# Optimization experiments

Measured on AMD Instinct MI355X. Metric: run time of the kernel, lower is better.

## Reference

```python
import math
import jax, jax.numpy as jnp
import numpy as np

B, S, D, H = 4, 2048, 1024, 16
HD = D // H
SAMPLING_FACTOR = 5.0


def setup_inputs() -> dict:
    key = jax.random.key(0)
    ks = jax.random.split(key, 6)
    std = 1.0 / math.sqrt(D)
    inp = {
        "x": jax.random.normal(ks[0], (B, S, D), dtype=jnp.float32),
        "Wq": jax.random.normal(ks[1], (D, D), dtype=jnp.float32) * std,
        "bq": jnp.zeros((D,), dtype=jnp.float32),
        "Wk": jax.random.normal(ks[2], (D, D), dtype=jnp.float32) * std,
        "bk": jnp.zeros((D,), dtype=jnp.float32),
        "Wv": jax.random.normal(ks[3], (D, D), dtype=jnp.float32) * std,
        "bv": jnp.zeros((D,), dtype=jnp.float32),
        "Wo": jax.random.normal(ks[4], (D, D), dtype=jnp.float32) * std,
        "bo": jnp.zeros((D,), dtype=jnp.float32),
        "sample_idx": jax.random.randint(ks[5], (S,), 0, S, dtype=jnp.int32),
    }
    return inp


def reference(x, Wq, bq, Wk, bk, Wv, bv, Wo, bo, sample_idx):
    batch, seq_len, d_model = x.shape
    scale = math.sqrt(HD)
    # u = number of top (active) queries; U_part = seq_len here (sampling saturates)
    u = max(1, min(seq_len, int(SAMPLING_FACTOR * math.log(seq_len + 1))))

    def proj(W, b):
        # [B,S,D] -> [B,H,S,hd]
        return (x @ W + b).reshape(batch, seq_len, H, HD).transpose(0, 2, 1, 3)

    Q = proj(Wq, bq)
    K = proj(Wk, bk)
    V = proj(Wv, bv)

    # sparsity measure over sampled keys (with replacement)
    K_sample = K[:, :, sample_idx, :]                     # [B,H,U,hd]
    scores_sample = jnp.einsum("bhsd,bhud->bhsu", Q, K_sample) / scale
    M = scores_sample.max(axis=-1) - scores_sample.mean(axis=-1)  # [B,H,S]

    _, top_idx = jax.lax.top_k(M, u)                      # [B,H,u]

    Q_reduce = jnp.take_along_axis(Q, top_idx[..., None], axis=2)  # [B,H,u,hd]
    attn_scores = jnp.einsum("bhud,bhsd->bhus", Q_reduce, K) / scale
    attn_probs = jax.nn.softmax(attn_scores, axis=-1)
    context = jnp.einsum("bhus,bhsd->bhud", attn_probs, V)        # [B,H,u,hd]

    # fill lazy queries with mean of V, scatter active-query contexts
    V_mean = V.mean(axis=2, keepdims=True)                # [B,H,1,hd]
    out = jnp.broadcast_to(V_mean, (batch, H, seq_len, HD))
    b_idx = jnp.arange(batch)[:, None, None]
    h_idx = jnp.arange(H)[None, :, None]
    out = out.at[b_idx, h_idx, top_idx].set(context)      # [B,H,S,hd]

    out = out.transpose(0, 2, 1, 3).reshape(batch, seq_len, d_model)
    return out @ Wo + bo
```

## Files before the change

### kernel.cpp

```cpp
#include <hip/hip_runtime.h>
#include <math.h>
#include <stdint.h>
#include <stddef.h>

#define BB 4
#define SS 2048
#define DD 1024
#define HH 16
#define HD 64
#define UU 38
#define BH (BB*HH)
#define NROWS (BB*SS)
#define QSZ (BB*HH*SS*HD)
#define NSPLIT 16
#define SPLEN (SS/NSPLIT)
#define QPAD 40

typedef unsigned short ushortT;
typedef unsigned int u32;
typedef __attribute__((ext_vector_type(8))) short bf16x8;
typedef __attribute__((ext_vector_type(4))) float f32x4;

static __device__ __forceinline__ ushortT f2bf(float f) {
  union { float f; unsigned int u; } v; v.f = f;
  unsigned int r = v.u + 0x7fffu + ((v.u >> 16) & 1u);
  return (ushortT)(r >> 16);
}
static __device__ __forceinline__ float bf2f(ushortT h) {
  union { unsigned int u; float f; } v; v.u = ((unsigned int)h) << 16; return v.f;
}
static __device__ __forceinline__ void gld16(const void* g, void* l) {
  __builtin_amdgcn_global_load_lds((const __attribute__((address_space(1))) u32*)g,
                                   (__attribute__((address_space(3))) u32*)l, 16, 0, 0);
}

__global__ __launch_bounds__(256) void split_x(
    const float* __restrict__ x, ushortT* __restrict__ xh, ushortT* __restrict__ xl)
{
  size_t i = ((size_t)blockIdx.x * 256 + threadIdx.x) * 8;
  float4 v0 = *(const float4*)&x[i];
  float4 v1 = *(const float4*)&x[i + 4];
  float fv[8] = {v0.x, v0.y, v0.z, v0.w, v1.x, v1.y, v1.z, v1.w};
  bf16x8 hv, lv;
#pragma unroll
  for (int j = 0; j < 8; ++j) {
    ushortT h = f2bf(fv[j]);
    hv[j] = (short)h;
    lv[j] = (short)f2bf(fv[j] - bf2f(h));
  }
  *(bf16x8*)&xh[i] = hv;
  *(bf16x8*)&xl[i] = lv;
}

__global__ __launch_bounds__(256) void splitT_kernel(
    const float* __restrict__ W, ushortT* __restrict__ WhT, ushortT* __restrict__ WlT)
{
  __shared__ float tile[64][65];
  const int t = threadIdx.x;
  const int bk = blockIdx.y * 64, bn = blockIdx.x * 64;
  const int rr = t >> 4, c4 = (t & 15) * 4;
#pragma unroll
  for (int p = 0; p < 4; ++p) {
    int row = rr + p * 16;
    float4 v = *(const float4*)&W[(size_t)(bk + row) * DD + bn + c4];
    tile[row][c4] = v.x; tile[row][c4+1] = v.y; tile[row][c4+2] = v.z; tile[row][c4+3] = v.w;
  }
  __syncthreads();
  const int n = t & 63, ks = (t >> 6) * 16;
  union { ushortT us[16]; uint4 q[2]; } hb, lb;
#pragma unroll
  for (int j = 0; j < 16; ++j) {
    float f = tile[ks + j][n];
    ushortT h = f2bf(f);
    hb.us[j] = h;
    lb.us[j] = f2bf(f - bf2f(h));
  }
  size_t o = ((size_t)(bn + n) * DD + (size_t)(bk + ks)) >> 3;
  ((uint4*)WhT)[o] = hb.q[0]; ((uint4*)WhT)[o + 1] = hb.q[1];
  ((uint4*)WlT)[o] = lb.q[0]; ((uint4*)WlT)[o + 1] = lb.q[1];
}

__global__ __launch_bounds__(256) void dedupe_kernel(
    const int* __restrict__ sidx, int* __restrict__ uidx, int* __restrict__ ucount)
{
  __shared__ unsigned bm[64];
  __shared__ int base[64];
  const int t = threadIdx.x;
  if (t < 64) bm[t] = 0;
  __syncthreads();
  for (int s = t; s < SS; s += 256) {
    int v = sidx[s];
    atomicOr(&bm[v >> 5], 1u << (v & 31));
  }
  __syncthreads();
  if (t < 64) {
    int c = __popc(bm[t]);
    int pre = c;
#pragma unroll
    for (int off = 1; off < 64; off <<= 1) {
      int o = __shfl_up(pre, off, 64);
      if (t >= off) pre += o;
    }
    base[t] = pre - c;
    if (t == 63) ucount[0] = pre;
  }
  __syncthreads();
  if (t < 64) {
    unsigned m = bm[t];
    int o = base[t];
    while (m) {
      int b = __ffs(m) - 1;
      uidx[o++] = t * 32 + b;
      m &= m - 1;
    }
  }
  __syncthreads();
  int total = ucount[0];
  int padded = (total + 127) & ~127;
  int first = uidx[0];
  for (int i = total + t; i < padded; i += 256) uidx[i] = first;
}

__global__ __launch_bounds__(256, 4) void gemm_qkv(
    const ushortT* __restrict__ Axh, const ushortT* __restrict__ Axl,
    const ushortT* __restrict__ WqhT, const ushortT* __restrict__ WqlT,
    const ushortT* __restrict__ WkhT, const ushortT* __restrict__ WklT,
    const ushortT* __restrict__ WvhT, const ushortT* __restrict__ WvlT,
    const float* __restrict__ bq, const float* __restrict__ bk, const float* __restrict__ bv,
    ushortT* __restrict__ Qhg, ushortT* __restrict__ Qlg,
    ushortT* __restrict__ Khg, ushortT* __restrict__ Klg,
    float* __restrict__ V)
{
  __shared__ ushortT As[128 * 64];
  __shared__ ushortT Bs[128 * 64];
  const int t = threadIdx.x;
  const int lin = blockIdx.x;
  const int xcd = lin & 7;
  const int idx = lin >> 3;
  const int msub = idx & 3;
  const int rest = idx >> 2;
  const int n_idx = rest % 24;
  const int half = rest / 24;
  const int m_loc = half * 4 + msub;
  const int m0 = (xcd * 8 + m_loc) * 128;
  const int p = n_idx >> 3;
  const int n0 = (n_idx & 7) * 128;
  const ushortT* Bh = (p == 0) ? WqhT : (p == 1) ? WkhT : WvhT;
  const ushortT* Bl = (p == 0) ? WqlT : (p == 1) ? WklT : WvlT;
  const float* bias = (p == 0) ? bq : (p == 1) ? bk : bv;
  const int lane = t & 63, w = t >> 6;
  const int wr = w >> 1, wc = w & 1;
  const int fr = lane & 15, fs = lane >> 4;
  const int srow = t >> 3, sslot = t & 7;
  f32x4 acc[4][4];
#pragma unroll
  for (int i = 0; i < 4; ++i)
#pragma unroll
    for (int j = 0; j < 4; ++j) acc[i][j] = (f32x4){0.f, 0.f, 0.f, 0.f};

  for (int kt = 0; kt < 48; ++kt) {
    const int seg = kt >> 4;
    const int rk0 = (kt & 15) * 64;
    const ushortT* a_src = (seg == 1) ? Axl : Axh;
    const ushortT* b_src = (seg == 2) ? Bl : Bh;
    __syncthreads();
#pragma unroll
    for (int is = 0; is < 4; ++is) {
      int row = is * 32 + srow;
      int soff = ((sslot ^ (row & 7)) * 8);
      int cb = (is * 256 + (t & 192)) * 8;
      gld16(&a_src[(size_t)(m0 + row) * DD + rk0 + soff], &As[cb]);
      gld16(&b_src[(size_t)(n0 + row) * DD + rk0 + soff], &Bs[cb]);
    }
    __syncthreads();
#pragma unroll
    for (int kk = 0; kk < 2; ++kk) {
      bf16x8 af[4], bf[4];
#pragma unroll
      for (int i = 0; i < 4; ++i) {
        int row = wr * 64 + i * 16 + fr;
        af[i] = *(const bf16x8*)&As[row * 64 + (((kk * 4 + fs) ^ (row & 7)) * 8)];
      }
#pragma unroll
      for (int j = 0; j < 4; ++j) {
        int row = wc * 64 + j * 16 + fr;
        bf[j] = *(const bf16x8*)&Bs[row * 64 + (((kk * 4 + fs) ^ (row & 7)) * 8)];
      }
#pragma unroll
      for (int i = 0; i < 4; ++i)
#pragma unroll
        for (int j = 0; j < 4; ++j)
          acc[i][j] = __builtin_amdgcn_mfma_f32_16x16x32_bf16(af[i], bf[j], acc[i][j], 0, 0, 0);
    }
  }
#pragma unroll
  for (int i = 0; i < 4; ++i) {
#pragma unroll
    for (int j = 0; j < 4; ++j) {
      int c = n0 + wc * 64 + j * 16 + fr;
      float bs = bias[c];
      int h = c >> 6, hd = c & 63;
#pragma unroll
      for (int r = 0; r < 4; ++r) {
        int m = m0 + wr * 64 + i * 16 + fs * 4 + r;
        int b = m >> 11, s = m & (SS - 1);
        size_t oidx = (((size_t)(b * HH + h)) * SS + s) * HD + hd;
        float val = acc[i][j][r] + bs;
        if (p == 2) {
          V[oidx] = val;
        } else {
          ushortT hv = f2bf(val);
          ushortT lv = f2bf(val - bf2f(hv));
          if (p == 0) { Qhg[oidx] = hv; Qlg[oidx] = lv; }
          else        { Khg[oidx] = hv; Klg[oidx] = lv; }
        }
      }
    }
  }
}

__global__ __launch_bounds__(256) void means_kernel(
    const ushortT* __restrict__ Khg, const ushortT* __restrict__ Klg,
    const float* __restrict__ V, const int* __restrict__ sidx,
    float* __restrict__ Kmean, float* __restrict__ Vmean)
{
  __shared__ float rk[4][64], rv[4][64];
  const int bh = blockIdx.x;
  const int t = threadIdx.x;
  const int d = t & 63, p = t >> 6;
  const float* Vb = V + (size_t)bh * SS * HD;
  float ka = 0.f, va = 0.f;
  for (int r = p * 512; r < (p + 1) * 512; ++r) {
    size_t ki = ((size_t)bh * SS + sidx[r]) * HD + d;
    ka += bf2f(Khg[ki]) + bf2f(Klg[ki]);
    va += Vb[(size_t)r * HD + d];
  }
  rk[p][d] = ka; rv[p][d] = va;
  __syncthreads();
  if (t < 64) {
    Kmean[bh * HD + t] = (rk[0][t] + rk[1][t] + rk[2][t] + rk[3][t]) * (1.0f / SS);
    Vmean[bh * HD + t] = (rv[0][t] + rv[1][t] + rv[2][t] + rv[3][t]) * (1.0f / SS);
  }
}

__global__ __launch_bounds__(256, 3) void m_mfma(
    const ushortT* __restrict__ Qhg, const ushortT* __restrict__ Qlg,
    const ushortT* __restrict__ Khg, const ushortT* __restrict__ Klg,
    const int* __restrict__ uidx, const int* __restrict__ ucount,
    const float* __restrict__ Kmean, float* __restrict__ M)
{
  __shared__ ushortT KhL[128 * 64], KlL[128 * 64];
  __shared__ float Mred[2][128];
  __shared__ float km[64];
  const int t = threadIdx.x;
  const int lin = blockIdx.x;
  const int swz = (lin & 7) * 128 + (lin >> 3);
  const int bh = swz >> 4;
  const int s0 = (swz & 15) * 128;
  const int lane = t & 63, w = t >> 6;
  const int wr = w >> 1, wc = w & 1;
  const int fr = lane & 15, fs = lane >> 4;
  if (t < 64) km[t] = Kmean[bh * HD + t];
  const int srow = t >> 3, sslot = t & 7;
  const int ntiles = (ucount[0] + 127) >> 7;
  const size_t qbase = (size_t)bh * SS + s0;
  float runmax[4][4];
#pragma unroll
  for (int i = 0; i < 4; ++i)
#pragma unroll
    for (int r = 0; r < 4; ++r) runmax[i][r] = -INFINITY;

  for (int ui = 0; ui < ntiles; ++ui) {
    __syncthreads();
#pragma unroll
    for (int is = 0; is < 4; ++is) {
      int row = is * 32 + srow;
      int gr = uidx[ui * 128 + row];
      int soff = ((sslot ^ (row & 7)) * 8);
      int cb = (is * 256 + (t & 192)) * 8;
      size_t ga = ((size_t)bh * SS + gr) * HD + soff;
      gld16(&Khg[ga], &KhL[cb]);
      gld16(&Klg[ga], &KlL[cb]);
    }
    __syncthreads();
    f32x4 acc[4][4];
#pragma unroll
    for (int i = 0; i < 4; ++i)
#pragma unroll
      for (int j = 0; j < 4; ++j) acc[i][j] = (f32x4){0.f, 0.f, 0.f, 0.f};
#pragma unroll
    for (int kk = 0; kk < 2; ++kk) {
      bf16x8 ah[4], al[4], bh[4], bl[4];
#pragma unroll
      for (int i = 0; i < 4; ++i) {
        size_t ga = (qbase + (size_t)(wr * 64 + i * 16 + fr)) * HD + kk * 32 + fs * 8;
        ah[i] = *(const bf16x8*)&Qhg[ga];
        al[i] = *(const bf16x8*)&Qlg[ga];
      }
#pragma unroll
      for (int j = 0; j < 4; ++j) {
        int row = wc * 64 + j * 16 + fr;
        int off = row * 64 + (((kk * 4 + fs) ^ (row & 7)) * 8);
        bh[j] = *(const bf16x8*)&KhL[off];
        bl[j] = *(const bf16x8*)&KlL[off];
      }
#pragma unroll
      for (int i = 0; i < 4; ++i)
#pragma unroll
        for (int j = 0; j < 4; ++j) {
          acc[i][j] = __builtin_amdgcn_mfma_f32_16x16x32_bf16(ah[i], bh[j], acc[i][j], 0, 0, 0);
          acc[i][j] = __builtin_amdgcn_mfma_f32_16x16x32_bf16(ah[i], bl[j], acc[i][j], 0, 0, 0);
          acc[i][j] = __builtin_amdgcn_mfma_f32_16x16x32_bf16(al[i], bh[j], acc[i][j], 0, 0, 0);
        }
    }
#pragma unroll
    for (int i = 0; i < 4; ++i)
#pragma unroll
      for (int j = 0; j < 4; ++j)
#pragma unroll
        for (int r = 0; r < 4; ++r) runmax[i][r] = fmaxf(runmax[i][r], acc[i][j][r]);
  }
#pragma unroll
  for (int i = 0; i < 4; ++i)
#pragma unroll
    for (int r = 0; r < 4; ++r) {
      float v = runmax[i][r];
      v = fmaxf(v, __shfl_xor(v, 1, 64));
      v = fmaxf(v, __shfl_xor(v, 2, 64));
      v = fmaxf(v, __shfl_xor(v, 4, 64));
      v = fmaxf(v, __shfl_xor(v, 8, 64));
      runmax[i][r] = v;
    }
  if (fr == 0) {
#pragma unroll
    for (int i = 0; i < 4; ++i)
#pragma unroll
      for (int r = 0; r < 4; ++r)
        Mred[wc][wr * 64 + i * 16 + fs * 4 + r] = runmax[i][r];
  }
  __syncthreads();
  if (t < 128) {
    float mx = fmaxf(Mred[0][t], Mred[1][t]);
    float md = 0.f;
    const ushortT* qh = &Qhg[(qbase + t) * HD];
    const ushortT* ql = &Qlg[(qbase + t) * HD];
#pragma unroll
    for (int k8 = 0; k8 < 8; ++k8) {
      bf16x8 hv = *(const bf16x8*)&qh[k8 * 8];
      bf16x8 lv = *(const bf16x8*)&ql[k8 * 8];
#pragma unroll
      for (int j = 0; j < 8; ++j)
        md += (bf2f((ushortT)hv[j]) + bf2f((ushortT)lv[j])) * km[k8 * 8 + j];
    }
    M[(size_t)bh * SS + s0 + t] = (mx - md) * 0.125f;
  }
}

__global__ __launch_bounds__(256) void topk_kernel(const float* __restrict__ M,
                                                   int* __restrict__ topi)
{
  __shared__ float rw[4];
  __shared__ int   ri4[4];
  __shared__ int   winner;
  const int t = threadIdx.x, bh = blockIdx.x;
  const int lane = t & 63, w = t >> 6;
  float v[8];
#pragma unroll
  for (int j = 0; j < 8; ++j) v[j] = M[(size_t)bh * SS + t + j * 256];
  for (int it = 0; it < UU; ++it) {
    float bv = v[0]; int bj = 0;
#pragma unroll
    for (int j = 1; j < 8; ++j) if (v[j] > bv) { bv = v[j]; bj = j; }
    int bs = t + bj * 256;
#pragma unroll
    for (int off = 32; off > 0; off >>= 1) {
      float ov = __shfl_xor(bv, off, 64);
      int os = __shfl_xor(bs, off, 64);
      if (ov > bv || (ov == bv && os < bs)) { bv = ov; bs = os; }
    }
    if (lane == 0) { rw[w] = bv; ri4[w] = bs; }
    __syncthreads();
    if (t == 0) {
      float fv = rw[0]; int fsx = ri4[0];
#pragma unroll
      for (int g = 1; g < 4; ++g)
        if (rw[g] > fv || (rw[g] == fv && ri4[g] < fsx)) { fv = rw[g]; fsx = ri4[g]; }
      topi[bh * UU + it] = fsx;
      winner = fsx;
    }
    __syncthreads();
    int wi = winner;
    if ((wi & 255) == t) {
      int jj = wi >> 8;
#pragma unroll
      for (int j = 0; j < 8; ++j) if (j == jj) v[j] = -INFINITY;
    }
  }
}

__global__ __launch_bounds__(256) void attn_flash(
    const ushortT* __restrict__ Qhg, const ushortT* __restrict__ Qlg,
    const ushortT* __restrict__ Khg, const ushortT* __restrict__ Klg,
    const float* __restrict__ V, const int* __restrict__ topi,
    float* __restrict__ pacc, float* __restrict__ pm, float* __restrict__ pl)
{
  __shared__ float Qt[64][68];
  __shared__ float KV[64][68];
  __shared__ float Ps[64][68];
  __shared__ float redA[16][64];
  __shared__ float redB[16][64];
  __shared__ float mrow[64], lrow[64], scl[64];
  const int t  = threadIdx.x;
  const int bh = blockIdx.x;
  const int sp = blockIdx.y;
  const float* Vb = V + (size_t)bh * SS * HD;
  if (t < 64) { mrow[t] = -INFINITY; lrow[t] = 0.f; }
  {
    int q = t >> 2, k4 = (t & 3) * 16;
    float fv[16];
#pragma unroll
    for (int e = 0; e < 16; ++e) fv[e] = 0.f;
    if (q < UU) {
      int qidx = topi[bh * UU + q];
      size_t ga = ((size_t)bh * SS + qidx) * HD + k4;
      bf16x8 h0 = *(const bf16x8*)&Qhg[ga];
      bf16x8 h1 = *(const bf16x8*)&Qhg[ga + 8];
      bf16x8 l0 = *(const bf16x8*)&Qlg[ga];
      bf16x8 l1 = *(const bf16x8*)&Qlg[ga + 8];
#pragma unroll
      for (int j = 0; j < 8; ++j) {
        fv[j]     = bf2f((ushortT)h0[j]) + bf2f((ushortT)l0[j]);
        fv[8 + j] = bf2f((ushortT)h1[j]) + bf2f((ushortT)l1[j]);
      }
    }
#pragma unroll
    for (int e = 0; e < 16; ++e) Qt[k4 + e][q] = fv[e];
  }
  const int q4 = (t & 15) * 4, j4g = (t >> 4) * 4, d4 = (t >> 4) * 4;
  const int lj = t >> 2, lk4 = (t & 3) * 16;
  float acc[4][4] = {};
  for (int s0 = sp * SPLEN; s0 < (sp + 1) * SPLEN; s0 += 64) {
    __syncthreads();
    {
      size_t ga = ((size_t)bh * SS + s0 + lj) * HD + lk4;
      bf16x8 h0 = *(const bf16x8*)&Khg[ga];
      bf16x8 h1 = *(const bf16x8*)&Khg[ga + 8];
      bf16x8 l0 = *(const bf16x8*)&Klg[ga];
      bf16x8 l1 = *(const bf16x8*)&Klg[ga + 8];
#pragma unroll
      for (int j = 0; j < 8; ++j) {
        KV[lk4 + j][lj]     = bf2f((ushortT)h0[j]) + bf2f((ushortT)l0[j]);
        KV[lk4 + 8 + j][lj] = bf2f((ushortT)h1[j]) + bf2f((ushortT)l1[j]);
      }
    }
    __syncthreads();
    float sacc[4][4] = {};
#pragma unroll 16
    for (int k = 0; k < 64; ++k) {
      float4 a = *(const float4*)&Qt[k][q4];
      float4 b = *(const float4*)&KV[k][j4g];
      sacc[0][0] += a.x*b.x; sacc[0][1] += a.x*b.y; sacc[0][2] += a.x*b.z; sacc[0][3] += a.x*b.w;
      sacc[1][0] += a.y*b.x; sacc[1][1] += a.y*b.y; sacc[1][2] += a.y*b.z; sacc[1][3] += a.y*b.w;
      sacc[2][0] += a.z*b.x; sacc[2][1] += a.z*b.y; sacc[2][2] += a.z*b.z; sacc[2][3] += a.z*b.w;
      sacc[3][0] += a.w*b.x; sacc[3][1] += a.w*b.y; sacc[3][2] += a.w*b.z; sacc[3][3] += a.w*b.w;
    }
#pragma unroll
    for (int i = 0; i < 4; ++i) {
      float mx = fmaxf(fmaxf(sacc[i][0], sacc[i][1]), fmaxf(sacc[i][2], sacc[i][3]));
      redA[t >> 4][q4 + i] = mx;
    }
    __syncthreads();
    if (t < 64) {
      float mx = redA[0][t];
#pragma unroll
      for (int g = 1; g < 16; ++g) mx = fmaxf(mx, redA[g][t]);
      float mn = fmaxf(mrow[t], mx * 0.125f);
      scl[t] = __expf(mrow[t] - mn);
      mrow[t] = mn;
    }
    __syncthreads();
    float4 vld[4];
#pragma unroll
    for (int i = 0; i < 4; ++i)
      vld[i] = *(const float4*)&Vb[(size_t)(s0 + lj) * HD + lk4 + 4 * i];
    float psum[4] = {};
#pragma unroll
    for (int i = 0; i < 4; ++i) {
#pragma unroll
      for (int j = 0; j < 4; ++j) {
        float e = __expf(sacc[i][j] * 0.125f - mrow[q4 + i]);
        Ps[j4g + j][q4 + i] = e;
        psum[i] += e;
      }
      redB[t >> 4][q4 + i] = psum[i];
    }
#pragma unroll
    for (int i = 0; i < 4; ++i)
      *(float4*)&KV[lj][lk4 + 4 * i] = vld[i];
    __syncthreads();
    if (t < 64) {
      float ts = redB[0][t];
#pragma unroll
      for (int g = 1; g < 16; ++g) ts += redB[g][t];
      lrow[t] = lrow[t] * scl[t] + ts;
    }
#pragma unroll
    for (int i = 0; i < 4; ++i) {
      float fsc = scl[q4 + i];
      acc[i][0] *= fsc; acc[i][1] *= fsc; acc[i][2] *= fsc; acc[i][3] *= fsc;
    }
#pragma unroll 16
    for (int j = 0; j < 64; ++j) {
      float4 a = *(const float4*)&Ps[j][q4];
      float4 b = *(const float4*)&KV[j][d4];
      acc[0][0] += a.x*b.x; acc[0][1] += a.x*b.y; acc[0][2] += a.x*b.z; acc[0][3] += a.x*b.w;
      acc[1][0] += a.y*b.x; acc[1][1] += a.y*b.y; acc[1][2] += a.y*b.z; acc[1][3] += a.y*b.w;
      acc[2][0] += a.z*b.x; acc[2][1] += a.z*b.y; acc[2][2] += a.z*b.z; acc[2][3] += a.z*b.w;
      acc[3][0] += a.w*b.x; acc[3][1] += a.w*b.y; acc[3][2] += a.w*b.z; acc[3][3] += a.w*b.w;
    }
  }
  const size_t pb = ((size_t)bh * NSPLIT + sp) * QPAD;
#pragma unroll
  for (int i = 0; i < 4; ++i) {
    int q = q4 + i;
    if (q < UU) {
#pragma unroll
      for (int j = 0; j < 4; ++j)
        pacc[(pb + q) * HD + d4 + j] = acc[i][j];
    }
  }
  if (t < UU) { pm[pb + t] = mrow[t]; pl[pb + t] = lrow[t]; }
}

__global__ __launch_bounds__(256) void attn_combine(
    const float* __restrict__ pacc, const float* __restrict__ pm,
    const float* __restrict__ pl, float* __restrict__ ctx)
{
  const int t  = threadIdx.x;
  const int bh = blockIdx.x;
  const int d = t & 63, qg = t >> 6;
  for (int q = qg; q < UU; q += 4) {
    float mv[NSPLIT];
    float ms = -INFINITY;
#pragma unroll
    for (int sp = 0; sp < NSPLIT; ++sp) {
      mv[sp] = pm[((size_t)bh * NSPLIT + sp) * QPAD + q];
      ms = fmaxf(ms, mv[sp]);
    }
    float l = 0.f, c = 0.f;
#pragma unroll
    for (int sp = 0; sp < NSPLIT; ++sp) {
      float wv = __expf(mv[sp] - ms);
      l += wv * pl[((size_t)bh * NSPLIT + sp) * QPAD + q];
      c += wv * pacc[(((size_t)bh * NSPLIT + sp) * QPAD + q) * HD + d];
    }
    ctx[((size_t)bh * UU + q) * HD + d] = c / l;
  }
}

__global__ __launch_bounds__(256) void base_kernel(
    const float* __restrict__ Vmean, const float* __restrict__ Wo,
    const float* __restrict__ bo, float* __restrict__ base)
{
  __shared__ float red[16][BB][16];
  const int t = threadIdx.x;
  const int cl = t & 15, kg = t >> 4;
  const int c = blockIdx.x * 16 + cl;
  float acc[BB] = {};
  for (int k = kg * 64; k < kg * 64 + 64; ++k) {
    float w = Wo[(size_t)k * DD + c];
#pragma unroll
    for (int b = 0; b < BB; ++b) acc[b] += Vmean[b * DD + k] * w;
  }
#pragma unroll
  for (int b = 0; b < BB; ++b) red[kg][b][cl] = acc[b];
  __syncthreads();
  if (t < 64) {
    int b = t >> 4, cc = blockIdx.x * 16 + (t & 15);
    float s = 0.f;
#pragma unroll
    for (int g = 0; g < 16; ++g) s += red[g][b][t & 15];
    base[b * DD + cc] = s + bo[cc];
  }
}

__global__ void fill_kernel(const float* __restrict__ base, float* __restrict__ out)
{
  size_t i = (size_t)blockIdx.x * 256 + threadIdx.x;
  float4 bv = ((const float4*)base)[(i >> 19) * 256 + (i & 255)];
  ((float4*)out)[i] = bv;
}

__global__ __launch_bounds__(256) void scatter_kernel(
    const float* __restrict__ ctx, const float* __restrict__ Vmean,
    const int* __restrict__ topi, const float* __restrict__ Wo,
    float* __restrict__ out)
{
  __shared__ float delta[64];
  const int t  = threadIdx.x;
  const int bh = blockIdx.x;
  const int u  = blockIdx.y;
  const int b = bh >> 4, h = bh & 15;
  const int s = topi[bh * UU + u];
  if (t < 64) delta[t] = ctx[((size_t)bh * UU + u) * HD + t] - Vmean[bh * HD + t];
  __syncthreads();
  float* orow = out + ((size_t)b * SS + s) * DD;
#pragma unroll
  for (int j = 0; j < 4; ++j) {
    int c = t + j * 256;
    float acc = 0.f;
#pragma unroll 8
    for (int d = 0; d < 64; ++d) acc += delta[d] * Wo[(size_t)(h * HD + d) * DD + c];
    atomicAdd(&orow[c], acc);
  }
}

extern "C" void kernel_launch(void* const* d_in, const int* in_sizes, int n_in,
                              void* d_out, int out_size, void* d_ws, size_t ws_size,
                              hipStream_t stream) {
  const float* x  = (const float*)d_in[0];
  const float* Wq = (const float*)d_in[1];
  const float* bq = (const float*)d_in[2];
  const float* Wk = (const float*)d_in[3];
  const float* bk = (const float*)d_in[4];
  const float* Wv = (const float*)d_in[5];
  const float* bv = (const float*)d_in[6];
  const float* Wo = (const float*)d_in[7];
  const float* bo = (const float*)d_in[8];
  const int* sidx = (const int*)d_in[9];
  float* out = (float*)d_out;

  float* f     = (float*)d_ws;
  float* V     = f;
  float* Kmean = f + (size_t)QSZ;
  float* Vmean = Kmean + BH * HD;
  float* Mbuf  = Vmean + BH * HD;
  float* base  = Mbuf + (size_t)BH * SS;
  float* ctx   = base + BB * DD;
  float* pacc  = ctx + (size_t)BH * UU * HD;
  float* pm    = pacc + (size_t)BH * NSPLIT * QPAD * HD;
  float* pl    = pm + (size_t)BH * NSPLIT * QPAD;
  int*   topi  = (int*)(pl + (size_t)BH * NSPLIT * QPAD);
  int*   uidx  = topi + 4096;
  int*   ucount= uidx + 4096;
  ushortT* usp = (ushortT*)(ucount + 64);
  ushortT* WqhT = usp;
  ushortT* WqlT = WqhT + (size_t)DD * DD;
  ushortT* WkhT = WqlT + (size_t)DD * DD;
  ushortT* WklT = WkhT + (size_t)DD * DD;
  ushortT* WvhT = WklT + (size_t)DD * DD;
  ushortT* WvlT = WvhT + (size_t)DD * DD;
  ushortT* xh   = WvlT + (size_t)DD * DD;
  ushortT* xl   = xh + (size_t)NROWS * DD;
  ushortT* Qhg  = xl + (size_t)NROWS * DD;
  ushortT* Qlg  = Qhg + (size_t)QSZ;
  ushortT* Khg  = Qlg + (size_t)QSZ;
  ushortT* Klg  = Khg + (size_t)QSZ;

  split_x<<<NROWS * DD / (256 * 8), 256, 0, stream>>>(x, xh, xl);
  dim3 gs(16, 16);
  splitT_kernel<<<gs, 256, 0, stream>>>(Wq, WqhT, WqlT);
  splitT_kernel<<<gs, 256, 0, stream>>>(Wk, WkhT, WklT);
  splitT_kernel<<<gs, 256, 0, stream>>>(Wv, WvhT, WvlT);
  dedupe_kernel<<<1, 256, 0, stream>>>(sidx, uidx, ucount);
  gemm_qkv<<<1536, 256, 0, stream>>>(xh, xl, WqhT, WqlT, WkhT, WklT, WvhT, WvlT,
                                     bq, bk, bv, Qhg, Qlg, Khg, Klg, V);
  means_kernel<<<BH, 256, 0, stream>>>(Khg, Klg, V, sidx, Kmean, Vmean);
  m_mfma<<<1024, 256, 0, stream>>>(Qhg, Qlg, Khg, Klg, uidx, ucount, Kmean, Mbuf);
  topk_kernel<<<BH, 256, 0, stream>>>(Mbuf, topi);
  attn_flash<<<dim3(BH, NSPLIT), 256, 0, stream>>>(Qhg, Qlg, Khg, Klg, V, topi, pacc, pm, pl);
  attn_combine<<<BH, 256, 0, stream>>>(pacc, pm, pl, ctx);
  base_kernel<<<DD / 16, 256, 0, stream>>>(Vmean, Wo, bo, base);
  fill_kernel<<<(NROWS * DD / 4) / 256, 256, 0, stream>>>(base, out);
  scatter_kernel<<<dim3(BH, UU), 256, 0, stream>>>(ctx, Vmean, topi, Wo, out);
}
```

Before: 438.1 us.

## Double-buffer QKV GEMM with 256x128 tiles and 512-thread blocks

Rewrites the QKV projection GEMM to use 256x128 output tiles with 8 waves per block, and halves the grid to match. LDS staging is split into half-K chunks, and the next tile's global-to-LDS loads are issued before the current chunk's MFMAs. Waits use counted vmcnt plus raw barriers, so load latency can overlap with compute. MFMA sections are wrapped in setprio to favour math waves. This uses more LDS per block and lowers occupancy, and the hand-counted waitcnt carries ordering risk.

Result: slower. 456.8 us (+4.3%).

```diff
diff --git a/kernel.cpp b/kernel.cpp
--- a/kernel.cpp
+++ b/kernel.cpp
@@ -15,6 +15,7 @@
 #define NSPLIT 16
 #define SPLEN (SS/NSPLIT)
 #define QPAD 40
+#define NT 48
 
 typedef unsigned short ushortT;
 typedef unsigned int u32;
@@ -121,7 +122,7 @@
   for (int i = total + t; i < padded; i += 256) uidx[i] = first;
 }
 
-__global__ __launch_bounds__(256, 4) void gemm_qkv(
+__global__ __launch_bounds__(512) void gemm_qkv(
     const ushortT* __restrict__ Axh, const ushortT* __restrict__ Axl,
     const ushortT* __restrict__ WqhT, const ushortT* __restrict__ WqlT,
     const ushortT* __restrict__ WkhT, const ushortT* __restrict__ WklT,
@@ -131,78 +132,99 @@
     ushortT* __restrict__ Khg, ushortT* __restrict__ Klg,
     float* __restrict__ V)
 {
-  __shared__ ushortT As[128 * 64];
-  __shared__ ushortT Bs[128 * 64];
+  __shared__ ushortT L[49152];
   const int t = threadIdx.x;
   const int lin = blockIdx.x;
   const int xcd = lin & 7;
   const int idx = lin >> 3;
-  const int msub = idx & 3;
-  const int rest = idx >> 2;
-  const int n_idx = rest % 24;
-  const int half = rest / 24;
-  const int m_loc = half * 4 + msub;
-  const int m0 = (xcd * 8 + m_loc) * 128;
+  const int m0 = (xcd * 4 + (idx & 3)) * 256;
+  const int n_idx = idx >> 2;
   const int p = n_idx >> 3;
-  const int n0 = (n_idx & 7) * 128;
+  const int n0g = (n_idx & 7) * 128;
   const ushortT* Bh = (p == 0) ? WqhT : (p == 1) ? WkhT : WvhT;
   const ushortT* Bl = (p == 0) ? WqlT : (p == 1) ? WklT : WvlT;
   const float* bias = (p == 0) ? bq : (p == 1) ? bk : bv;
-  const int lane = t & 63, w = t >> 6;
-  const int wr = w >> 1, wc = w & 1;
+  const int lane = t & 63, wid = t >> 6;
+  const int wrm = wid >> 1, wcn = wid & 1;
   const int fr = lane & 15, fs = lane >> 4;
-  const int srow = t >> 3, sslot = t & 7;
+  const int srow = t >> 2, sc = t & 3;
+  const int wbase = (t & ~63) * 8;
+
   f32x4 acc[4][4];
 #pragma unroll
   for (int i = 0; i < 4; ++i)
 #pragma unroll
     for (int j = 0; j < 4; ++j) acc[i][j] = (f32x4){0.f, 0.f, 0.f, 0.f};
 
-  for (int kt = 0; kt < 48; ++kt) {
-    const int seg = kt >> 4;
-    const int rk0 = (kt & 15) * 64;
-    const ushortT* a_src = (seg == 1) ? Axl : Axh;
-    const ushortT* b_src = (seg == 2) ? Bl : Bh;
-    __syncthreads();
-#pragma unroll
-    for (int is = 0; is < 4; ++is) {
-      int row = is * 32 + srow;
-      int soff = ((sslot ^ (row & 7)) * 8);
-      int cb = (is * 256 + (t & 192)) * 8;
-      gld16(&a_src[(size_t)(m0 + row) * DD + rk0 + soff], &As[cb]);
-      gld16(&b_src[(size_t)(n0 + row) * DD + rk0 + soff], &Bs[cb]);
-    }
-    __syncthreads();
-#pragma unroll
-    for (int kk = 0; kk < 2; ++kk) {
-      bf16x8 af[4], bf[4];
-#pragma unroll
-      for (int i = 0; i < 4; ++i) {
-        int row = wr * 64 + i * 16 + fr;
-        af[i] = *(const bf16x8*)&As[row * 64 + (((kk * 4 + fs) ^ (row & 7)) * 8)];
-      }
-#pragma unroll
-      for (int j = 0; j < 4; ++j) {
-        int row = wc * 64 + j * 16 + fr;
-        bf[j] = *(const bf16x8*)&Bs[row * 64 + (((kk * 4 + fs) ^ (row & 7)) * 8)];
-      }
-#pragma unroll
-      for (int i = 0; i < 4; ++i)
-#pragma unroll
-        for (int j = 0; j < 4; ++j)
-          acc[i][j] = __builtin_amdgcn_mfma_f32_16x16x32_bf16(af[i], bf[j], acc[i][j], 0, 0, 0);
-    }
-  }
+  auto stageA = [&](int Ts, int kk) {
+    const ushortT* a_src = ((Ts >> 4) == 1) ? Axl : Axh;
+    int k0 = (Ts & 15) * 64 + kk * 32;
+    int slot = ((Ts & 1) * 2 + kk) * 8192;
+#pragma unroll
+    for (int rd = 0; rd < 2; ++rd) {
+      int row = rd * 128 + srow;
+      int cdat = sc ^ ((row >> 1) & 3);
+      gld16(&a_src[(size_t)(m0 + row) * DD + k0 + cdat * 8],
+            &L[slot + rd * 4096 + wbase]);
+    }
+  };
+  auto stageB = [&](int Ts, int kk) {
+    const ushortT* b_src = ((Ts >> 4) == 2) ? Bl : Bh;
+    int k0 = (Ts & 15) * 64 + kk * 32;
+    int slot = 32768 + ((Ts & 1) * 2 + kk) * 4096;
+    int cdat = sc ^ ((srow >> 1) & 3);
+    gld16(&b_src[(size_t)(n0g + srow) * DD + k0 + cdat * 8], &L[slot + wbase]);
+  };
+  auto compute = [&](int pb, int kk) {
+    int aslot = (pb * 2 + kk) * 8192;
+    int bslot = 32768 + (pb * 2 + kk) * 4096;
+    bf16x8 a[4], b[4];
+#pragma unroll
+    for (int i = 0; i < 4; ++i) {
+      int row = wrm * 64 + i * 16 + fr;
+      a[i] = *(const bf16x8*)&L[aslot + row * 32 + ((fs ^ ((row >> 1) & 3)) * 8)];
+    }
+#pragma unroll
+    for (int j = 0; j < 4; ++j) {
+      int row = wcn * 64 + j * 16 + fr;
+      b[j] = *(const bf16x8*)&L[bslot + row * 32 + ((fs ^ ((row >> 1) & 3)) * 8)];
+    }
+    __builtin_amdgcn_s_setprio(1);
+#pragma unroll
+    for (int i = 0; i < 4; ++i)
+#pragma unroll
+      for (int j = 0; j < 4; ++j)
+        acc[i][j] = __builtin_amdgcn_mfma_f32_16x16x32_bf16(a[i], b[j], acc[i][j], 0, 0, 0);
+    __builtin_amdgcn_s_setprio(0);
+  };
+
+  stageA(0, 0); stageB(0, 0);
+  stageA(0, 1); stageB(0, 1);
+  asm volatile("s_waitcnt vmcnt(3)" ::: "memory");
+  __builtin_amdgcn_s_barrier();
+
+  for (int T = 0; T < NT; ++T) {
+    const int pb = T & 1;
+    if (T + 1 < NT) { stageA(T + 1, 0); stageB(T + 1, 0); }
+    compute(pb, 0);
+    asm volatile("s_waitcnt vmcnt(3)" ::: "memory");
+    __builtin_amdgcn_s_barrier();
+    if (T + 1 < NT) { stageA(T + 1, 1); stageB(T + 1, 1); }
+    compute(pb, 1);
+    asm volatile("s_waitcnt vmcnt(3)" ::: "memory");
+    __builtin_amdgcn_s_barrier();
+  }
+
 #pragma unroll
   for (int i = 0; i < 4; ++i) {
 #pragma unroll
     for (int j = 0; j < 4; ++j) {
-      int c = n0 + wc * 64 + j * 16 + fr;
+      int c = n0g + wcn * 64 + j * 16 + fr;
       float bs = bias[c];
       int h = c >> 6, hd = c & 63;
 #pragma unroll
       for (int r = 0; r < 4; ++r) {
-        int m = m0 + wr * 64 + i * 16 + fs * 4 + r;
+        int m = m0 + wrm * 64 + i * 16 + fs * 4 + r;
         int b = m >> 11, s = m & (SS - 1);
         size_t oidx = (((size_t)(b * HH + h)) * SS + s) * HD + hd;
         float val = acc[i][j][r] + bs;
@@ -663,8 +685,8 @@
   splitT_kernel<<<gs, 256, 0, stream>>>(Wk, WkhT, WklT);
   splitT_kernel<<<gs, 256, 0, stream>>>(Wv, WvhT, WvlT);
   dedupe_kernel<<<1, 256, 0, stream>>>(sidx, uidx, ucount);
-  gemm_qkv<<<1536, 256, 0, stream>>>(xh, xl, WqhT, WqlT, WkhT, WklT, WvhT, WvlT,
-                                     bq, bk, bv, Qhg, Qlg, Khg, Klg, V);
+  gemm_qkv<<<768, 512, 0, stream>>>(xh, xl, WqhT, WqlT, WkhT, WklT, WvhT, WvlT,
+                                    bq, bk, bv, Qhg, Qlg, Khg, Klg, V);
   means_kernel<<<BH, 256, 0, stream>>>(Khg, Klg, V, sidx, Kmean, Vmean);
   m_mfma<<<1024, 256, 0, stream>>>(Qhg, Qlg, Khg, Klg, uidx, ucount, Kmean, Mbuf);
   topk_kernel<<<BH, 256, 0, stream>>>(Mbuf, topi);
```
